# Optimization experiments

Hardware: AMD Instinct MI355X
Metric: run time of the kernel (lower is better)

The kernel has to match this reference:

```python
import jax, jax.numpy as jnp
import numpy as np

TEMP = 0.01  # temperature_att_sc


def grid_sample_bilinear(img, grid):
    """torch.nn.functional.grid_sample, mode='bilinear', padding_mode='zeros',
    align_corners=False. img: (B,C,H,W); grid: (B,Hg,Wg,2) with (x,y) coords."""
    B, C, H, W = img.shape
    gx, gy = grid[..., 0], grid[..., 1]            # (B,Hg,Wg)
    ix = ((gx + 1.0) * W - 1.0) * 0.5              # unnormalize (align_corners=False)
    iy = ((gy + 1.0) * H - 1.0) * 0.5
    ix0 = jnp.floor(ix); iy0 = jnp.floor(iy)
    ix1 = ix0 + 1.0;     iy1 = iy0 + 1.0
    wx1 = ix - ix0; wx0 = 1.0 - wx1
    wy1 = iy - iy0; wy0 = 1.0 - wy1
    flat = img.reshape(B, C, H * W)
    Hg, Wg = gx.shape[1], gx.shape[2]

    def gather(iy_, ix_):
        valid = (ix_ >= 0) & (ix_ <= W - 1) & (iy_ >= 0) & (iy_ <= H - 1)
        ixc = jnp.clip(ix_, 0, W - 1).astype(jnp.int32)
        iyc = jnp.clip(iy_, 0, H - 1).astype(jnp.int32)
        idx = (iyc * W + ixc).reshape(B, 1, Hg * Wg)
        vals = jnp.take_along_axis(flat, jnp.broadcast_to(idx, (B, C, Hg * Wg)), axis=2)
        vals = vals.reshape(B, C, Hg, Wg)
        return vals * valid[:, None, :, :].astype(img.dtype)

    out = (gather(iy0, ix0) * (wy0 * wx0)[:, None]
         + gather(iy0, ix1) * (wy0 * wx1)[:, None]
         + gather(iy1, ix0) * (wy1 * wx0)[:, None]
         + gather(iy1, ix1) * (wy1 * wx1)[:, None])
    return out


def setup_inputs() -> dict:
    key = jax.random.key(0)
    ks = jax.random.split(key, 16)
    B, S, D = 256, 197, 768
    H60 = 60
    std = 0.02
    inp = {
        "x": jax.random.normal(ks[0], (B, S, D), dtype=jnp.float32),
        "mask": jnp.zeros((B, S), dtype=jnp.float32),
        "Wq": jax.random.normal(ks[1], (D, D), dtype=jnp.float32) * std,
        "bq": jnp.zeros((D,), dtype=jnp.float32),
        "Wk": jax.random.normal(ks[2], (D, D), dtype=jnp.float32) * std,
        "bk": jnp.zeros((D,), dtype=jnp.float32),
        "Wv": jax.random.normal(ks[3], (D, D), dtype=jnp.float32) * std,
        "bv": jnp.zeros((D,), dtype=jnp.float32),
        "W1": jax.random.normal(ks[4], (H60, 2 * D), dtype=jnp.float32) * std,
        "b1": jnp.zeros((H60,), dtype=jnp.float32),
        "W2": jax.random.normal(ks[5], (H60, H60), dtype=jnp.float32) * std,
        "b2": jnp.zeros((H60,), dtype=jnp.float32),
        "W3": jax.random.normal(ks[6], (2, H60), dtype=jnp.float32) * std,
        "b3": jnp.zeros((2,), dtype=jnp.float32),
    }
    return inp


def reference(x, mask, Wq, bq, Wk, bk, Wv, bv, W1, b1, W2, b2, W3, b3):
    B, S, D = x.shape
    G = int(np.sqrt(S))  # grid_dim; S = G*G + 1 (class token)
    q = jnp.einsum('bsd,ed->bse', x, Wq) + bq
    k = jnp.einsum('bsd,ed->bse', x, Wk) + bk
    v = jnp.einsum('bsd,ed->bse', x, Wv) + bv
    k_nc = k[:, 1:, :]          # (B, G*G, D)
    v_nc = v[:, 1:, :]
    q_nc = q[:, 1:, :]
    k_img = jnp.transpose(k_nc, (0, 2, 1)).reshape(B, D, G, G)
    v_img = jnp.transpose(v_nc, (0, 2, 1)).reshape(B, D, G, G)
    # key_net_2D MLP -> per-patch sampling offsets in [0,1]
    h = jnp.concatenate((q_nc, k_nc), axis=2)       # (B, G*G, 2D)
    h = jax.nn.relu(jnp.einsum('bse,fe->bsf', h, W1) + b1)
    h = jax.nn.relu(jnp.einsum('bse,fe->bsf', h, W2) + b2)
    sample = jax.nn.sigmoid(jnp.einsum('bse,fe->bsf', h, W3) + b3)  # (B, G*G, 2)
    sample_x = sample[:, :, 0:1]
    sample_y = sample[:, :, 1:2]
    grid = jnp.concatenate((sample_x, sample_y), axis=1).reshape(B, G, G, 2)
    sk = grid_sample_bilinear(k_img, grid)          # (B, D, G, G)
    sv = grid_sample_bilinear(v_img, grid)
    sk = jnp.transpose(sk.reshape(B, D, G * G), (0, 2, 1))  # (B, G*G, D)
    sv = jnp.transpose(sv.reshape(B, D, G * G), (0, 2, 1))
    cls = jnp.ones((B, 1, D), dtype=x.dtype)
    sk = jnp.concatenate((cls, sk), axis=1)         # (B, S, D)
    sv = jnp.concatenate((cls, sv), axis=1)
    scores = jnp.sum(sk * q, axis=-1)               # (B, S)
    attention = jax.nn.sigmoid(TEMP * scores)[:, :, None] * sv
    return attention
```

## Files before the change

kernel.cpp:

```cpp
#include <hip/hip_runtime.h>
#include <hip/hip_bf16.h>
#include <stdint.h>

#define TEMP 0.01f

typedef __attribute__((ext_vector_type(8))) short short8;
typedef __attribute__((ext_vector_type(4))) float f32x4;
typedef __attribute__((ext_vector_type(2))) float f32x2;

__device__ __forceinline__ ushort f2bf(float f) {
  union { float f; uint32_t u; } c; c.f = f;
  uint32_t u = c.u;
  uint32_t r = (u + 0x7FFFu + ((u >> 16) & 1u)) >> 16;
  return (ushort)r;
}
__device__ __forceinline__ float bf2f(ushort h) {
  union { uint32_t u; float f; } c; c.u = ((uint32_t)h) << 16;
  return c.f;
}

__device__ __forceinline__ void async16(void* lds, const void* g) {
  __builtin_amdgcn_global_load_lds(
      (const __attribute__((address_space(1))) uint32_t*)g,
      (__attribute__((address_space(3))) uint32_t*)lds,
      16, 0, 0);
}

__global__ __launch_bounds__(256) void convert_all(
    const float* __restrict__ X, ushort* __restrict__ Xb,
    const float* __restrict__ Wq, const float* __restrict__ Wk, const float* __restrict__ Wv,
    const float* __restrict__ bq, const float* __restrict__ bk, const float* __restrict__ bv,
    const float* __restrict__ W1, const float* __restrict__ b1,
    ushort* __restrict__ wqkv, ushort* __restrict__ w1p,
    float* __restrict__ biasq, float* __restrict__ b1p) {
  int idx = blockIdx.x * 256 + threadIdx.x;
  int stride = gridDim.x * 256;
  for (int i = idx; i < 9682944; i += stride) {
    float4 f = ((const float4*)X)[i];
    ushort4 u;
    u.x = f2bf(f.x); u.y = f2bf(f.y); u.z = f2bf(f.z); u.w = f2bf(f.w);
    ((ushort4*)Xb)[i] = u;
  }
  for (int i = idx; i < 2304 * 768; i += stride) {
    int row = i / 768;
    float v = (row < 768) ? Wq[i] : (row < 1536) ? Wk[i - 768 * 768] : Wv[i - 1536 * 768];
    wqkv[i] = f2bf(v);
  }
  for (int i = idx; i < 64 * 1536; i += stride) {
    int row = i / 1536;
    w1p[i] = f2bf(row < 60 ? W1[i] : 0.f);
  }
  for (int i = idx; i < 2304; i += stride)
    biasq[i] = (i < 768) ? bq[i] : (i < 1536) ? bk[i - 768] : bv[i - 1536];
  for (int i = idx; i < 64; i += stride)
    b1p[i] = (i < 60) ? b1[i] : 0.f;
}

#define STAGE(LDSBASE, SRC, OFF)                                          \
  async16(smem + (LDSBASE) + ldsW, (SRC) + (OFF));                        \
  async16(smem + (LDSBASE) + 8192 + ldsW, (SRC) + 64 * 1536 + (OFF))

#define RDA4(BASE, F0)                                                                   \
  _Pragma("unroll") for (int f = 0; f < 4; ++f) {                                        \
    a[f][0] = *(const short8*)(smem + (BASE) + aRow + ((F0) + f) * 2048 + c0);           \
    a[f][1] = *(const short8*)(smem + (BASE) + aRow + ((F0) + f) * 2048 + c1);           \
  }
#define RDB2(BASE, G0)                                                                   \
  _Pragma("unroll") for (int g = 0; g < 2; ++g) {                                        \
    b[(G0) + g][0] = *(const short8*)(smem + (BASE) + bRow + ((G0) + g) * 2048 + c0);    \
    b[(G0) + g][1] = *(const short8*)(smem + (BASE) + bRow + ((G0) + g) * 2048 + c1);    \
  }
#define MF16(F0, G0)                                                                     \
  _Pragma("unroll") for (int f = 0; f < 4; ++f)                                          \
  _Pragma("unroll") for (int g = 0; g < 2; ++g) {                                        \
    acc[(F0) + f][(G0) + g] = __builtin_amdgcn_mfma_f32_16x16x32_bf16(                   \
        a[f][0], b[(G0) + g][0], acc[(F0) + f][(G0) + g], 0, 0, 0);                      \
    acc[(F0) + f][(G0) + g] = __builtin_amdgcn_mfma_f32_16x16x32_bf16(                   \
        a[f][1], b[(G0) + g][1], acc[(F0) + f][(G0) + g], 0, 0, 0);                      \
  }
#define PH_OPEN                                          \
  __builtin_amdgcn_s_barrier();                          \
  asm volatile("s_waitcnt lgkmcnt(0)" ::: "memory");     \
  __builtin_amdgcn_s_setprio(1);
#define PH_CLOSE                                         \
  __builtin_amdgcn_s_setprio(0);                         \
  __builtin_amdgcn_s_barrier();

__device__ __forceinline__ void tilecoord(int orig, int& m0, int& n0) {
  int xcd = orig & 7, idx = orig >> 3;
  int nw = (xcd < 5 ? xcd * 222 : 1110 + (xcd - 5) * 221) + idx;
  m0 = (nw / 9) * 256;
  n0 = (nw % 9) * 256;
}

__global__ __launch_bounds__(512, 1) void gemm_qkv(const ushort* __restrict__ Xb,
                                                   const ushort* __restrict__ Wb,
                                                   const float* __restrict__ bias,
                                                   ushort* __restrict__ QKV) {
  __shared__ char smem[131072];
  const int tid = threadIdx.x;
  const int lane = tid & 63;
  const int wv = tid >> 6;
  const int wr = wv >> 2;
  const int wc = wv & 3;
  const int lmod = lane & 15, ldiv = lane >> 4;
  const int bid = blockIdx.x;
  const int ntiles = (1772 - bid) / 256 + 1;

  const int srow = tid >> 3;
  const int scol = (((tid & 7) ^ (srow & 7)) << 4);
  const int ldsW = wv << 10;

  const int aRow = (wr * 128 + lmod) * 128;
  const int bRow = (wc * 64 + lmod) * 128;
  const int c0 = (ldiv * 16) ^ ((lmod & 7) << 4);
  const int c1 = (64 + ldiv * 16) ^ ((lmod & 7) << 4);

  const int AE = 0, AO = 32768, BE = 65536, BO = 98304;

  int m0, n0;
  tilecoord(bid, m0, n0);
  const char* aS = (const char*)Xb + (size_t)(m0 + srow) * 1536 + scol;
  const char* bS = (const char*)Wb + (size_t)(n0 + srow) * 1536 + scol;

  f32x4 acc[8][4] = {};

  STAGE(AE, aS, 0);
  STAGE(AE + 16384, aS + 128 * 1536, 0);
  STAGE(BE, bS, 0);
  STAGE(BE + 16384, bS + 128 * 1536, 0);
  STAGE(AO, aS, 128);
  asm volatile("s_waitcnt vmcnt(2)" ::: "memory");
  __builtin_amdgcn_s_barrier();

  for (int t = 0;; ++t) {
    const bool lastT = (t == ntiles - 1);
    int m0n = 0, n0n = 0;
    const char* aS2 = aS;
    const char* bS2 = bS;
    if (!lastT) {
      tilecoord(bid + 256 * (t + 1), m0n, n0n);
      aS2 = (const char*)Xb + (size_t)(m0n + srow) * 1536 + scol;
      bS2 = (const char*)Wb + (size_t)(n0n + srow) * 1536 + scol;
    }

    for (int i = 0; i < 6; ++i) {
      const int kb1 = i * 256 + 128;
      const bool ib = (i == 5);
      const bool stg = !(ib && lastT);
      const char* pA = ib ? aS2 : aS;
      const char* pB = ib ? bS2 : bS;
      const int kA = ib ? 0 : i * 256 + 256;

      short8 a[4][2], b[4][2];
      RDA4(AE, 0); RDB2(BE, 0);
      STAGE(AO + 16384, aS + 128 * 1536, kb1);
      PH_OPEN; MF16(0, 0); PH_CLOSE;
      RDB2(BE, 2);
      STAGE(BO, bS, kb1);
      PH_OPEN; MF16(0, 2); PH_CLOSE;
      RDA4(AE, 4);
      STAGE(BO + 16384, bS + 128 * 1536, kb1);
      PH_OPEN; MF16(4, 0); PH_CLOSE;
      if (stg) { STAGE(AE, pA, kA); }
      PH_OPEN; MF16(4, 2);
      __builtin_amdgcn_s_setprio(0);
      if (stg) { asm volatile("s_waitcnt vmcnt(2)" ::: "memory"); }
      else     { asm volatile("s_waitcnt vmcnt(0)" ::: "memory"); }
      __builtin_amdgcn_s_barrier();
      RDA4(AO, 0); RDB2(BO, 0);
      if (stg) { STAGE(AE + 16384, pA + 128 * 1536, kA); }
      PH_OPEN; MF16(0, 0); PH_CLOSE;
      RDB2(BO, 2);
      if (stg) { STAGE(BE, pB, kA); }
      PH_OPEN; MF16(0, 2); PH_CLOSE;
      RDA4(AO, 4);
      if (stg) { STAGE(BE + 16384, pB + 128 * 1536, kA); }
      PH_OPEN; MF16(4, 0); PH_CLOSE;
      if (stg) { STAGE(AO, pA, kA + 128); }
      PH_OPEN; MF16(4, 2);
      __builtin_amdgcn_s_setprio(0);
      if (stg) { asm volatile("s_waitcnt vmcnt(2)" ::: "memory"); }
      __builtin_amdgcn_s_barrier();
    }

#pragma unroll
    for (int f = 0; f < 8; ++f) {
      int row = m0 + wr * 128 + f * 16 + ldiv * 4;
#pragma unroll
      for (int g = 0; g < 4; ++g) {
        int col = n0 + wc * 64 + g * 16 + lmod;
        float bs = bias[col];
#pragma unroll
        for (int rr = 0; rr < 4; ++rr)
          QKV[(size_t)(row + rr) * 2304 + col] = f2bf(acc[f][g][rr] + bs);
      }
    }
    if (lastT) break;
#pragma unroll
    for (int f = 0; f < 8; ++f)
#pragma unroll
      for (int g = 0; g < 4; ++g)
        acc[f][g] = f32x4{0.f, 0.f, 0.f, 0.f};
    m0 = m0n; n0 = n0n; aS = aS2; bS = bS2;
  }
}

__global__ __launch_bounds__(256) void gemm_mlp(const ushort* __restrict__ QKV,
                                                const ushort* __restrict__ W1p,
                                                const float* __restrict__ b1p,
                                                const float* __restrict__ W2,
                                                const float* __restrict__ b2,
                                                const float* __restrict__ W3,
                                                const float* __restrict__ b3,
                                                float* __restrict__ SAMPLE) {
  __shared__ char smem[32032];
  float* sW2 = (float*)(smem + 16896);
  float* sW3 = (float*)(smem + 31296);
  float* sb2 = (float*)(smem + 31776);
  float* sb3 = (float*)(smem + 32016);
  const int tid = threadIdx.x;
  const int lane = tid & 63;
  const int wv = tid >> 6;
  const int p0 = blockIdx.x * 128;
  const int lmod = lane & 15, ldiv = lane >> 4;

  for (int i = tid; i < 3600; i += 256) sW2[i] = W2[i];
  for (int i = tid; i < 120; i += 256) sW3[i] = W3[i];
  if (tid < 60) sb2[tid] = b2[tid];
  if (tid < 2) sb3[tid] = b3[tid];

  f32x4 acc[2][4] = {};
  const ushort* As = (const ushort*)smem;
  const ushort* Bs = (const ushort*)(smem + 8192);

  const int r = tid >> 2, cb = (tid & 3) * 16;
  int p_a = p0 + r;
  int p_b = p0 + 64 + r;
  int grow_a = (p_a / 196) * 197 + 1 + (p_a % 196);
  int grow_b = (p_b / 196) * 197 + 1 + (p_b % 196);
  const char* gA0 = (const char*)QKV + (size_t)grow_a * 4608 + cb;
  const char* gA1 = (const char*)QKV + (size_t)grow_b * 4608 + cb;
  const char* gB = (const char*)W1p + (size_t)r * 3072 + cb;

  for (int k0 = 0; k0 < 1536; k0 += 32) {
    int kb = k0 * 2;
    async16(smem + wv * 1024,        gA0 + kb);
    async16(smem + 4096 + wv * 1024, gA1 + kb);
    async16(smem + 8192 + wv * 1024, gB + kb);
    __syncthreads();

    short8 a[2], b[4];
    a[0] = *(const short8*)(As + (wv * 32 + lmod) * 32 + ldiv * 8);
    a[1] = *(const short8*)(As + (wv * 32 + 16 + lmod) * 32 + ldiv * 8);
#pragma unroll
    for (int j = 0; j < 4; ++j)
      b[j] = *(const short8*)(Bs + (j * 16 + lmod) * 32 + ldiv * 8);
#pragma unroll
    for (int i = 0; i < 2; ++i)
#pragma unroll
      for (int j = 0; j < 4; ++j)
        acc[i][j] = __builtin_amdgcn_mfma_f32_16x16x32_bf16(a[i], b[j], acc[i][j], 0, 0, 0);
    __syncthreads();
  }

  ushort* Hs = (ushort*)smem;
#pragma unroll
  for (int i = 0; i < 2; ++i) {
    int lrow = wv * 32 + i * 16 + ldiv * 4;
#pragma unroll
    for (int j = 0; j < 4; ++j) {
      int col = j * 16 + lmod;
      float bs = b1p[col];
#pragma unroll
      for (int rr = 0; rr < 4; ++rr) {
        float v = fmaxf(acc[i][j][rr] + bs, 0.f);
        Hs[(lrow + rr) * 66 + col] = f2bf(v);
      }
    }
  }
  __syncthreads();

  const int plocal = tid >> 1;
  const int half = tid & 1;
  const uint32_t* hrow = (const uint32_t*)(Hs + plocal * 66);
  float h[60];
#pragma unroll
  for (int i = 0; i < 30; ++i) {
    uint32_t u = hrow[i];
    h[2 * i] = bf2f((ushort)(u & 0xffffu));
    h[2 * i + 1] = bf2f((ushort)(u >> 16));
  }
  float s0 = 0.f, s1 = 0.f;
  const int obase = half * 30;
  for (int oo = 0; oo < 30; ++oo) {
    int o = obase + oo;
    float a = sb2[o];
    const float4* wrow = (const float4*)(sW2 + o * 60);
#pragma unroll
    for (int k = 0; k < 15; ++k) {
      float4 w4 = wrow[k];
      a += h[4 * k] * w4.x + h[4 * k + 1] * w4.y + h[4 * k + 2] * w4.z + h[4 * k + 3] * w4.w;
    }
    a = fmaxf(a, 0.f);
    s0 += a * sW3[o];
    s1 += a * sW3[60 + o];
  }
  s0 += __shfl_xor(s0, 1, 64);
  s1 += __shfl_xor(s1, 1, 64);
  if (half == 0) {
    int p = p0 + plocal;
    SAMPLE[2 * p]     = 1.f / (1.f + __expf(-(s0 + sb3[0])));
    SAMPLE[2 * p + 1] = 1.f / (1.f + __expf(-(s1 + sb3[1])));
  }
}

__global__ __launch_bounds__(256) void sample_attn(const ushort* __restrict__ QKV,
                                                   const float* __restrict__ SAMPLE,
                                                   float* __restrict__ OUT) {
  int tid = threadIdx.x, lane = tid & 63, wv = tid >> 6;
  int orig = blockIdx.x;
  int nw = (orig & 7) * 1576 + (orig >> 3);
  int pos = nw * 4 + wv;
  int b = pos / 197, s = pos % 197;

  const uint32_t* qrow = (const uint32_t*)(QKV + (size_t)pos * 2304);
  float qv[12];
#pragma unroll
  for (int j = 0; j < 6; ++j) {
    uint32_t u = qrow[lane + j * 64];
    qv[2 * j] = bf2f((ushort)(u & 0xffffu));
    qv[2 * j + 1] = bf2f((ushort)(u >> 16));
  }

  float sk[12], sv[12];
#pragma unroll
  for (int j = 0; j < 12; ++j) { sk[j] = 0.f; sv[j] = 0.f; }

  if (s == 0) {
#pragma unroll
    for (int j = 0; j < 12; ++j) { sk[j] = 1.f; sv[j] = 1.f; }
  } else {
    int g = s - 1;
    int t0 = 2 * g, t1 = 2 * g + 1;
    const float* smp = SAMPLE + (size_t)b * 392;
    float gx = (t0 < 196) ? smp[2 * t0] : smp[2 * (t0 - 196) + 1];
    float gy = (t1 < 196) ? smp[2 * t1] : smp[2 * (t1 - 196) + 1];
    float ix = ((gx + 1.f) * 14.f - 1.f) * 0.5f;
    float iy = ((gy + 1.f) * 14.f - 1.f) * 0.5f;
    float fx0 = floorf(ix), fy0 = floorf(iy);
    float wx1 = ix - fx0, wx0 = 1.f - wx1;
    float wy1 = iy - fy0, wy0 = 1.f - wy1;
    int x0 = (int)fx0, x1 = x0 + 1, y0 = (int)fy0, y1 = y0 + 1;
    float w[4] = {wy0 * wx0, wy0 * wx1, wy1 * wx0, wy1 * wx1};
    int xs[4] = {x0, x1, x0, x1};
    int ys[4] = {y0, y0, y1, y1};
#pragma unroll
    for (int c = 0; c < 4; ++c) {
      bool valid = (xs[c] >= 0) && (xs[c] <= 13) && (ys[c] >= 0) && (ys[c] <= 13);
      float wc = valid ? w[c] : 0.f;
      int xc = min(max(xs[c], 0), 13);
      int yc = min(max(ys[c], 0), 13);
      const uint32_t* krow =
          (const uint32_t*)(QKV + ((size_t)(b * 197 + 1 + yc * 14 + xc) * 2304 + 768));
      const uint32_t* vrow = krow + 384;
#pragma unroll
      for (int j = 0; j < 6; ++j) {
        uint32_t ku = krow[lane + j * 64];
        uint32_t vu = vrow[lane + j * 64];
        sk[2 * j]     += wc * bf2f((ushort)(ku & 0xffffu));
        sk[2 * j + 1] += wc * bf2f((ushort)(ku >> 16));
        sv[2 * j]     += wc * bf2f((ushort)(vu & 0xffffu));
        sv[2 * j + 1] += wc * bf2f((ushort)(vu >> 16));
      }
    }
  }

  float part = 0.f;
#pragma unroll
  for (int j = 0; j < 12; ++j) part += sk[j] * qv[j];
#pragma unroll
  for (int m = 1; m < 64; m <<= 1) part += __shfl_xor(part, m, 64);
  float sig = 1.f / (1.f + __expf(-TEMP * part));

  float* orow = OUT + (size_t)pos * 768;
#pragma unroll
  for (int j = 0; j < 6; ++j) {
    f32x2 o;
    o.x = sig * sv[2 * j];
    o.y = sig * sv[2 * j + 1];
    __builtin_nontemporal_store(o, (f32x2*)(orow + 2 * lane + 128 * j));
  }
}

extern "C" void kernel_launch(void* const* d_in, const int* in_sizes, int n_in,
                              void* d_out, int out_size, void* d_ws, size_t ws_size,
                              hipStream_t stream) {
  const float* x  = (const float*)d_in[0];
  const float* Wq = (const float*)d_in[2];
  const float* bq = (const float*)d_in[3];
  const float* Wk = (const float*)d_in[4];
  const float* bk = (const float*)d_in[5];
  const float* Wv = (const float*)d_in[6];
  const float* bv = (const float*)d_in[7];
  const float* W1 = (const float*)d_in[8];
  const float* b1 = (const float*)d_in[9];
  const float* W2 = (const float*)d_in[10];
  const float* b2 = (const float*)d_in[11];
  const float* W3 = (const float*)d_in[12];
  const float* b3 = (const float*)d_in[13];
  float* out = (float*)d_out;

  char* ws = (char*)d_ws;
  ushort* x_bf = (ushort*)ws;   ws += 77463552;
  ushort* qkv = (ushort*)ws;    ws += 232390656;
  ushort* wqkv = (ushort*)ws;   ws += 3538944;
  ushort* w1p = (ushort*)ws;    ws += 196608;
  float* biasq = (float*)ws;    ws += 9216;
  float* b1p = (float*)ws;      ws += 256;
  float* sample = (float*)ws;   ws += 401408;

  convert_all<<<2048, 256, 0, stream>>>(x, x_bf, Wq, Wk, Wv, bq, bk, bv, W1, b1,
                                        wqkv, w1p, biasq, b1p);
  gemm_qkv<<<256, 512, 0, stream>>>(x_bf, wqkv, biasq, qkv);
  gemm_mlp<<<392, 256, 0, stream>>>(qkv, w1p, b1p, W2, b2, W3, b3, sample);
  sample_attn<<<12608, 256, 0, stream>>>(qkv, sample, out);
}
```

Before: 337.7 us.

## Double-buffer LDS fragment registers to overlap reads with MFMA in QKV GEMM

Restructures the QKV GEMM inner loop to keep two sets of A/B register fragments (a0/a1, b0/b1), so LDS reads for the next MFMA quadrant are issued while the current quadrant computes. It uses partial lgkmcnt waits with sched_barrier instead of full waits, and shifts the staging schedule: the AO upper half is prefetched one step earlier, including in the prologue. The aim is to hide LDS read latency behind MFMA work, at the cost of more VGPRs and a more fragile barrier and wait ordering.

```diff
diff --git a/kernel.cpp b/kernel.cpp
--- a/kernel.cpp
+++ b/kernel.cpp
@@ -60,31 +60,30 @@
   async16(smem + (LDSBASE) + ldsW, (SRC) + (OFF));                        \
   async16(smem + (LDSBASE) + 8192 + ldsW, (SRC) + 64 * 1536 + (OFF))
 
-#define RDA4(BASE, F0)                                                                   \
+#define RD_A(DST, BASE, F0)                                                              \
   _Pragma("unroll") for (int f = 0; f < 4; ++f) {                                        \
-    a[f][0] = *(const short8*)(smem + (BASE) + aRow + ((F0) + f) * 2048 + c0);           \
-    a[f][1] = *(const short8*)(smem + (BASE) + aRow + ((F0) + f) * 2048 + c1);           \
-  }
-#define RDB2(BASE, G0)                                                                   \
+    DST[f][0] = *(const short8*)(smem + (BASE) + aRow + ((F0) + f) * 2048 + c0);         \
+    DST[f][1] = *(const short8*)(smem + (BASE) + aRow + ((F0) + f) * 2048 + c1);         \
+  }
+#define RD_B(DST, BASE, G0)                                                              \
   _Pragma("unroll") for (int g = 0; g < 2; ++g) {                                        \
-    b[(G0) + g][0] = *(const short8*)(smem + (BASE) + bRow + ((G0) + g) * 2048 + c0);    \
-    b[(G0) + g][1] = *(const short8*)(smem + (BASE) + bRow + ((G0) + g) * 2048 + c1);    \
-  }
-#define MF16(F0, G0)                                                                     \
+    DST[g][0] = *(const short8*)(smem + (BASE) + bRow + ((G0) + g) * 2048 + c0);         \
+    DST[g][1] = *(const short8*)(smem + (BASE) + bRow + ((G0) + g) * 2048 + c1);         \
+  }
+#define MFQ(F0, G0, A, B)                                                                \
   _Pragma("unroll") for (int f = 0; f < 4; ++f)                                          \
   _Pragma("unroll") for (int g = 0; g < 2; ++g) {                                        \
     acc[(F0) + f][(G0) + g] = __builtin_amdgcn_mfma_f32_16x16x32_bf16(                   \
-        a[f][0], b[(G0) + g][0], acc[(F0) + f][(G0) + g], 0, 0, 0);                      \
+        A[f][0], B[g][0], acc[(F0) + f][(G0) + g], 0, 0, 0);                             \
     acc[(F0) + f][(G0) + g] = __builtin_amdgcn_mfma_f32_16x16x32_bf16(                   \
-        a[f][1], b[(G0) + g][1], acc[(F0) + f][(G0) + g], 0, 0, 0);                      \
-  }
-#define PH_OPEN                                          \
-  __builtin_amdgcn_s_barrier();                          \
-  asm volatile("s_waitcnt lgkmcnt(0)" ::: "memory");     \
-  __builtin_amdgcn_s_setprio(1);
-#define PH_CLOSE                                         \
-  __builtin_amdgcn_s_setprio(0);                         \
-  __builtin_amdgcn_s_barrier();
+        A[f][1], B[g][1], acc[(F0) + f][(G0) + g], 0, 0, 0);                             \
+  }
+#define WAITK(N)                                                                         \
+  asm volatile("s_waitcnt lgkmcnt(" #N ")" ::: "memory");                                \
+  __builtin_amdgcn_sched_barrier(0)
+#define BAR __builtin_amdgcn_s_barrier()
+#define PRIO1 __builtin_amdgcn_s_setprio(1)
+#define PRIO0 __builtin_amdgcn_s_setprio(0)
 
 __device__ __forceinline__ void tilecoord(int orig, int& m0, int& n0) {
   int xcd = orig & 7, idx = orig >> 3;
@@ -124,14 +123,17 @@
   const char* bS = (const char*)Wb + (size_t)(n0 + srow) * 1536 + scol;
 
   f32x4 acc[8][4] = {};
+  short8 a0[4][2], a1[4][2], b0[2][2], b1[2][2];
 
   STAGE(AE, aS, 0);
   STAGE(AE + 16384, aS + 128 * 1536, 0);
   STAGE(BE, bS, 0);
   STAGE(BE + 16384, bS + 128 * 1536, 0);
   STAGE(AO, aS, 128);
-  asm volatile("s_waitcnt vmcnt(2)" ::: "memory");
-  __builtin_amdgcn_s_barrier();
+  STAGE(AO + 16384, aS + 128 * 1536, 128);
+  asm volatile("s_waitcnt vmcnt(4)" ::: "memory");
+  BAR;
+  RD_A(a0, AE, 0); RD_B(b0, BE, 0);
 
   for (int t = 0;; ++t) {
     const bool lastT = (t == ntiles - 1);
@@ -145,43 +147,55 @@
     }
 
     for (int i = 0; i < 6; ++i) {
-      const int kb1 = i * 256 + 128;
       const bool ib = (i == 5);
       const bool stg = !(ib && lastT);
       const char* pA = ib ? aS2 : aS;
       const char* pB = ib ? bS2 : bS;
-      const int kA = ib ? 0 : i * 256 + 256;
-
-      short8 a[4][2], b[4][2];
-      RDA4(AE, 0); RDB2(BE, 0);
-      STAGE(AO + 16384, aS + 128 * 1536, kb1);
-      PH_OPEN; MF16(0, 0); PH_CLOSE;
-      RDB2(BE, 2);
+      const int kE = ib ? 0 : i * 256 + 256;
+      const int kO = ib ? 128 : i * 256 + 384;
+      const int kb1 = i * 256 + 128;
+
+      RD_B(b1, BE, 2);
       STAGE(BO, bS, kb1);
-      PH_OPEN; MF16(0, 2); PH_CLOSE;
-      RDA4(AE, 4);
+      BAR; WAITK(4);
+      PRIO1; MFQ(0, 0, a0, b0); PRIO0;
+      BAR;
+      RD_A(a1, AE, 4);
       STAGE(BO + 16384, bS + 128 * 1536, kb1);
-      PH_OPEN; MF16(4, 0); PH_CLOSE;
-      if (stg) { STAGE(AE, pA, kA); }
-      PH_OPEN; MF16(4, 2);
-      __builtin_amdgcn_s_setprio(0);
+      BAR; WAITK(8);
+      PRIO1; MFQ(0, 2, a0, b1); PRIO0;
+      BAR;
+      if (stg) { STAGE(AE, pA, kE); }
+      BAR; WAITK(0);
+      PRIO1; MFQ(4, 0, a1, b0); PRIO0;
       if (stg) { asm volatile("s_waitcnt vmcnt(2)" ::: "memory"); }
       else     { asm volatile("s_waitcnt vmcnt(0)" ::: "memory"); }
-      __builtin_amdgcn_s_barrier();
-      RDA4(AO, 0); RDB2(BO, 0);
-      if (stg) { STAGE(AE + 16384, pA + 128 * 1536, kA); }
-      PH_OPEN; MF16(0, 0); PH_CLOSE;
-      RDB2(BO, 2);
-      if (stg) { STAGE(BE, pB, kA); }
-      PH_OPEN; MF16(0, 2); PH_CLOSE;
-      RDA4(AO, 4);
-      if (stg) { STAGE(BE + 16384, pB + 128 * 1536, kA); }
-      PH_OPEN; MF16(4, 0); PH_CLOSE;
-      if (stg) { STAGE(AO, pA, kA + 128); }
-      PH_OPEN; MF16(4, 2);
-      __builtin_amdgcn_s_setprio(0);
+      BAR;
+      RD_A(a0, AO, 0); RD_B(b0, BO, 0);
+      if (stg) { STAGE(AE + 16384, pA + 128 * 1536, kE); }
+      BAR;
+      PRIO1; MFQ(4, 2, a1, b1); PRIO0;
+      BAR;
+      RD_B(b1, BO, 2);
+      if (stg) { STAGE(BE, pB, kE); }
+      BAR; WAITK(4);
+      PRIO1; MFQ(0, 0, a0, b0); PRIO0;
+      BAR;
+      RD_A(a1, AO, 4);
+      if (stg) { STAGE(BE + 16384, pB + 128 * 1536, kE); }
+      BAR; WAITK(8);
+      PRIO1; MFQ(0, 2, a0, b1); PRIO0;
+      BAR;
+      if (stg) { STAGE(AO, pA, kO); }
+      BAR; WAITK(0);
+      PRIO1; MFQ(4, 0, a1, b0); PRIO0;
       if (stg) { asm volatile("s_waitcnt vmcnt(2)" ::: "memory"); }
-      __builtin_amdgcn_s_barrier();
+      BAR;
+      if (stg) { RD_A(a0, AE, 0); RD_B(b0, BE, 0); }
+      if (stg) { STAGE(AO + 16384, pA + 128 * 1536, kO); }
+      BAR;
+      PRIO1; MFQ(4, 2, a1, b1); PRIO0;
+      BAR;
     }
 
 #pragma unroll
```

Measured after the change: 459.2 us. +36.0%, slower.
